# Kernel tuning notes

Measured on AMD Instinct MI355X. Metric: run time of the kernel, lower is better.

## Reference

```python
import jax, jax.numpy as jnp
import numpy as np

B = 2048      # env batch (graphs)
A = 8         # agents per graph (fully connected)
N = B * A     # total nodes
DIN = 192     # raw obs dim
HD = 256      # h_dim (base MLP)
MD = 256      # mem_dim (GRU)
GD = 128      # gnn_dim (per-head GATv2 out, concat=False -> head mean)
H = 4         # GAT heads
NA = 20       # n_actions
ED = 3        # edge_dim


def setup_inputs() -> dict:
    key = jax.random.key(0)
    ks = jax.random.split(key, 16)
    # fully-connected directed graph per group of A agents, no self loops
    s, d = np.meshgrid(np.arange(A), np.arange(A), indexing='ij')
    mask = s != d
    s = s[mask]; d = d[mask]                     # [A*(A-1)]
    off = (np.arange(B) * A)[:, None]
    src = (off + s[None, :]).reshape(-1)
    dst = (off + d[None, :]).reshape(-1)
    edge_index = jnp.asarray(np.stack([src, dst]), dtype=jnp.int32)  # [2, E]
    E = src.shape[0]
    p = lambda k, sh: jax.random.normal(ks[k], sh, jnp.float32) * 0.02
    return {
        'inputs': jax.random.normal(ks[0], (N, DIN), jnp.float32),
        'hidden_states': jax.random.normal(ks[1], (N, MD), jnp.float32) * 0.1,
        'edge_index': edge_index,
        'edge_attr': jax.random.uniform(ks[2], (E, ED), jnp.float32),
        # base MLP (2 layers: Linear+ReLU+LayerNorm)
        'W1': p(3, (DIN, HD)), 'b1': jnp.zeros(HD), 'g1': jnp.ones(HD), 'be1': jnp.zeros(HD),
        'W2': p(4, (HD, HD)),  'b2': jnp.zeros(HD), 'g2': jnp.ones(HD), 'be2': jnp.zeros(HD),
        # GRUCell
        'Wih': p(5, (3 * MD, HD)), 'Whh': p(6, (3 * MD, MD)),
        'bih': jnp.zeros(3 * MD), 'bhh': jnp.zeros(3 * MD),
        # GATv2Conv (edge_dim=3, heads=4, concat=False, residual)
        'Wl': p(7, (MD, H * GD)), 'bl': jnp.zeros(H * GD),
        'Wr': p(8, (MD, H * GD)), 'br': jnp.zeros(H * GD),
        'att': p(9, (H, GD)),
        'We': p(10, (ED, H * GD)),
        'Wres': p(11, (MD, GD)),
        'bg': jnp.zeros(GD),
        # head: LayerNorm + Linear
        'lng': jnp.ones(GD), 'lnb': jnp.zeros(GD),
        'Wout': p(12, (GD, NA)), 'bout': jnp.zeros(NA),
    }


def _ln(x, g, b):
    mu = jnp.mean(x, -1, keepdims=True)
    xc = x - mu
    v = jnp.mean(xc * xc, -1, keepdims=True)
    return xc * jax.lax.rsqrt(v + 1e-5) * g + b


def _fwd(inputs, hidden_states, edge_attr, edge_index,
         W1, b1, g1, be1, W2, b2, g2, be2,
         Wih, Whh, bih, bhh,
         Wl, bl, Wr, br, att, We, Wres, bg,
         lng, lnb, Wout, bout):
    src, dst = edge_index[0], edge_index[1]
    # ---- base MLP encode ----
    x = _ln(jax.nn.relu(inputs @ W1 + b1), g1, be1)
    x = _ln(jax.nn.relu(x @ W2 + b2), g2, be2)          # [N, HD]
    # ---- SimpleConv(aggr='mean', combine_root='self_loop') ----
    s = jax.ops.segment_sum(x[src], dst, num_segments=N) + x
    deg = jax.ops.segment_sum(jnp.ones(src.shape[0], x.dtype), dst, num_segments=N) + 1.0
    x = s / deg[:, None]                                 # [N, HD]
    # ---- GRUCell ----
    gi = x @ Wih.T + bih
    gh = hidden_states @ Whh.T + bhh
    ir, iz, inn = jnp.split(gi, 3, -1)
    hr, hz, hn = jnp.split(gh, 3, -1)
    r = jax.nn.sigmoid(ir + hr)
    z = jax.nn.sigmoid(iz + hz)
    n = jnp.tanh(inn + r * hn)
    h = (1.0 - z) * n + z * hidden_states                # [N, MD]
    # ---- GATv2Conv (add self loops, edge_attr fill='mean') ----
    loop = jnp.arange(N, dtype=src.dtype)
    sf = jnp.concatenate([src, loop])
    df = jnp.concatenate([dst, loop])
    ea = jnp.concatenate([edge_attr, jnp.broadcast_to(edge_attr.mean(0), (N, ED))], 0)
    xl = (h @ Wl + bl).reshape(N, H, GD)
    xr = (h @ Wr + br).reshape(N, H, GD)
    m = xl[sf] + xr[df] + (ea @ We).reshape(-1, H, GD)   # [Ef, H, GD]
    m = jnp.where(m > 0, m, 0.2 * m)                     # leaky_relu(0.2)
    logits = jnp.einsum('ehc,hc->eh', m, att)            # [Ef, H]
    mx = jax.ops.segment_max(logits, df, num_segments=N)
    ex = jnp.exp(logits - mx[df])
    den = jax.ops.segment_sum(ex, df, num_segments=N)
    alpha = ex / (den[df] + 1e-16)                       # segment softmax
    out = jax.ops.segment_sum(xl[sf] * alpha[..., None], df, num_segments=N)
    out = out.mean(1) + h @ Wres + bg                    # head mean + residual + bias
    zg = jax.nn.relu(out)                                # [N, GD]
    # ---- action head ----
    q = _ln(zg, lng, lnb) @ Wout + bout                  # [N, NA]
    return q, h


def reference(inputs, hidden_states, edge_index, edge_attr,
              W1, b1, g1, be1, W2, b2, g2, be2,
              Wih, Whh, bih, bhh,
              Wl, bl, Wr, br, att, We, Wres, bg,
              lng, lnb, Wout, bout):
    return _fwd(inputs, hidden_states, edge_attr, edge_index,
                W1, b1, g1, be1, W2, b2, g2, be2,
                Wih, Whh, bih, bhh,
                Wl, bl, Wr, br, att, We, Wres, bg,
                lng, lnb, Wout, bout)
```

## Files before the change

### kernel.cpp

```cpp
#include <hip/hip_runtime.h>
#include <hip/hip_bf16.h>

constexpr int NB  = 2048;
constexpr int AG  = 8;
constexpr int NN  = NB * AG;
constexpr int DIN = 192;
constexpr int HD  = 256;
constexpr int MD  = 256;
constexpr int GD  = 128;
constexpr int NA  = 20;
constexpr int NE  = NB * AG * (AG - 1);

typedef __attribute__((ext_vector_type(8))) short bfrag8;
typedef __attribute__((ext_vector_type(4))) float f32x4;

#define MFMA16(a, b, c) __builtin_amdgcn_mfma_f32_16x16x32_bf16((a), (b), (c), 0, 0, 0)

__device__ __forceinline__ float bf2f(__hip_bfloat16 x) { return __bfloat162float(x); }
__device__ __forceinline__ __hip_bfloat16 f2bf(float x) { return __float2bfloat16(x); }
__device__ __forceinline__ short f2bs(float x) {
    __hip_bfloat16 b = __float2bfloat16(x);
    return *reinterpret_cast<short*>(&b);
}
__device__ __forceinline__ bfrag8 ldf(const __hip_bfloat16* p) { return *(const bfrag8*)p; }
__device__ __forceinline__ bfrag8 ldf32(const float* p) {
    const f32x4 a = *(const f32x4*)p;
    const f32x4 b = *(const f32x4*)(p + 4);
    bfrag8 r;
    r[0] = f2bs(a[0]); r[1] = f2bs(a[1]); r[2] = f2bs(a[2]); r[3] = f2bs(a[3]);
    r[4] = f2bs(b[0]); r[5] = f2bs(b[1]); r[6] = f2bs(b[2]); r[7] = f2bs(b[3]);
    return r;
}
__device__ __forceinline__ float sigmf(float x) { return 1.f / (1.f + __expf(-x)); }
__device__ __forceinline__ float blo(unsigned u) { return __uint_as_float(u << 16); }
__device__ __forceinline__ float bhi(unsigned u) { return __uint_as_float(u & 0xffff0000u); }

__global__ __launch_bounds__(256) void k_prep(
    const float* __restrict__ W1, const float* __restrict__ W2,
    const float* __restrict__ Wih, const float* __restrict__ Whh,
    const float* __restrict__ Wl, const float* __restrict__ bl,
    const float* __restrict__ Wr, const float* __restrict__ br,
    const float* __restrict__ Wres, const float* __restrict__ Wout,
    __hip_bfloat16* __restrict__ W1T, __hip_bfloat16* __restrict__ W2T,
    __hip_bfloat16* __restrict__ WihB, __hip_bfloat16* __restrict__ WhhB,
    __hip_bfloat16* __restrict__ WcatT, float* __restrict__ WoutTf,
    float* __restrict__ bcat)
{
    int i = blockIdx.x * 256 + threadIdx.x;
    if (i < 49152) { int o = i / 192, c = i % 192; W1T[i] = f2bf(W1[c * 256 + o]); return; }
    i -= 49152;
    if (i < 65536) { int o = i >> 8, c = i & 255; W2T[i] = f2bf(W2[c * 256 + o]); return; }
    i -= 65536;
    if (i < 196608) { WihB[i] = f2bf(Wih[i]); return; }
    i -= 196608;
    if (i < 196608) { WhhB[i] = f2bf(Whh[i]); return; }
    i -= 196608;
    if (i < 294912) {
        int o = i >> 8, c = i & 255;
        float v;
        if (o < 512)       v = Wl[c * 512 + o];
        else if (o < 1024) v = Wr[c * 512 + (o - 512)];
        else               v = Wres[c * 128 + (o - 1024)];
        WcatT[i] = f2bf(v); return;
    }
    i -= 294912;
    if (i < 2560) { int o = i >> 7, c = i & 127; WoutTf[i] = Wout[c * 20 + o]; return; }
    i -= 2560;
    if (i < 1152) {
        float v = 0.f;
        if (i < 512) v = bl[i]; else if (i < 1024) v = br[i - 512];
        bcat[i] = v;
    }
}

__global__ __launch_bounds__(256) void k_easum1(const float* __restrict__ ea,
                                                float* __restrict__ partials)
{
    __shared__ float sw[4][3];
    const int b = blockIdx.x, tid = threadIdx.x;
    float a0 = 0.f, a1 = 0.f, a2 = 0.f;
#pragma unroll
    for (int k = 0; k < 7; k++) {
        int e = b * 1792 + k * 256 + tid;
        a0 += ea[e * 3 + 0];
        a1 += ea[e * 3 + 1];
        a2 += ea[e * 3 + 2];
    }
#pragma unroll
    for (int off = 1; off < 64; off <<= 1) {
        a0 += __shfl_xor(a0, off); a1 += __shfl_xor(a1, off); a2 += __shfl_xor(a2, off);
    }
    if ((tid & 63) == 0) { sw[tid >> 6][0] = a0; sw[tid >> 6][1] = a1; sw[tid >> 6][2] = a2; }
    __syncthreads();
    if (tid == 0) {
        partials[b * 3 + 0] = sw[0][0] + sw[1][0] + sw[2][0] + sw[3][0];
        partials[b * 3 + 1] = sw[0][1] + sw[1][1] + sw[2][1] + sw[3][1];
        partials[b * 3 + 2] = sw[0][2] + sw[1][2] + sw[2][2] + sw[3][2];
    }
}

__global__ void k_easum2(const float* __restrict__ partials, float* __restrict__ ea_mean)
{
    int t = threadIdx.x;
    if (t < 3) {
        float s = 0.f;
        for (int i = 0; i < 64; i++) s += partials[i * 3 + t];
        ea_mean[t] = s * (1.f / NE);
    }
}

__global__ __launch_bounds__(256) void k_encode(
    const float* __restrict__ in,
    const __hip_bfloat16* __restrict__ W1T,
    const float* __restrict__ b1, const float* __restrict__ g1, const float* __restrict__ be1,
    const __hip_bfloat16* __restrict__ W2T,
    const float* __restrict__ b2, const float* __restrict__ g2, const float* __restrict__ be2,
    __hip_bfloat16* __restrict__ xm)
{
    __shared__ float sf[16][257];
    __shared__ alignas(16) __hip_bfloat16 sb[16][264];
    const int tid = threadIdx.x;
    const int lane = tid & 63, w = tid >> 6;
    const int r = lane & 15, q = lane >> 4;
    const int m0 = blockIdx.x * 16;

    f32x4 acc[4];
#pragma unroll
    for (int i = 0; i < 4; i++) acc[i] = (f32x4){0.f, 0.f, 0.f, 0.f};

    {
        const float* ap = in + (size_t)(m0 + r) * DIN + q * 8;
#pragma unroll
        for (int kb = 0; kb < 6; kb++) {
            bfrag8 af = ldf32(ap + kb * 32);
#pragma unroll
            for (int i = 0; i < 4; i++) {
                int t = w * 4 + i;
                bfrag8 bfv = ldf(W1T + (size_t)(t * 16 + r) * DIN + kb * 32 + q * 8);
                acc[i] = MFMA16(af, bfv, acc[i]);
            }
        }
    }
#pragma unroll
    for (int i = 0; i < 4; i++) {
        int col = (w * 4 + i) * 16 + r;
        float bias = b1[col];
#pragma unroll
        for (int reg = 0; reg < 4; reg++)
            sf[q * 4 + reg][col] = fmaxf(acc[i][reg] + bias, 0.f);
    }
    __syncthreads();
    {
        int rowi = tid >> 4, c16 = tid & 15;
        float vals[16]; float s = 0.f, s2 = 0.f;
#pragma unroll
        for (int j = 0; j < 16; j++) { float v = sf[rowi][c16 + 16 * j]; vals[j] = v; s += v; s2 += v * v; }
#pragma unroll
        for (int off = 1; off < 16; off <<= 1) { s += __shfl_xor(s, off); s2 += __shfl_xor(s2, off); }
        float mean = s * (1.f / HD);
        float var = fmaxf(s2 * (1.f / HD) - mean * mean, 0.f);
        float rs = rsqrtf(var + 1e-5f);
#pragma unroll
        for (int j = 0; j < 16; j++) {
            int col = c16 + 16 * j;
            sb[rowi][col] = f2bf((vals[j] - mean) * rs * g1[col] + be1[col]);
        }
    }
    __syncthreads();

#pragma unroll
    for (int i = 0; i < 4; i++) acc[i] = (f32x4){0.f, 0.f, 0.f, 0.f};
    {
        const __hip_bfloat16* ap = &sb[r][0];
#pragma unroll
        for (int kb = 0; kb < 8; kb++) {
            bfrag8 af = ldf(ap + kb * 32 + q * 8);
#pragma unroll
            for (int i = 0; i < 4; i++) {
                int t = w * 4 + i;
                bfrag8 bfv = ldf(W2T + (size_t)(t * 16 + r) * HD + kb * 32 + q * 8);
                acc[i] = MFMA16(af, bfv, acc[i]);
            }
        }
    }
    __syncthreads();
#pragma unroll
    for (int i = 0; i < 4; i++) {
        int col = (w * 4 + i) * 16 + r;
        float bias = b2[col];
#pragma unroll
        for (int reg = 0; reg < 4; reg++)
            sf[q * 4 + reg][col] = fmaxf(acc[i][reg] + bias, 0.f);
    }
    __syncthreads();
    {
        int rowi = tid >> 4, c16 = tid & 15;
        float vals[16]; float s = 0.f, s2 = 0.f;
#pragma unroll
        for (int j = 0; j < 16; j++) { float v = sf[rowi][c16 + 16 * j]; vals[j] = v; s += v; s2 += v * v; }
#pragma unroll
        for (int off = 1; off < 16; off <<= 1) { s += __shfl_xor(s, off); s2 += __shfl_xor(s2, off); }
        float mean = s * (1.f / HD);
        float var = fmaxf(s2 * (1.f / HD) - mean * mean, 0.f);
        float rs = rsqrtf(var + 1e-5f);
#pragma unroll
        for (int j = 0; j < 16; j++) {
            int col = c16 + 16 * j;
            sb[rowi][col] = f2bf((vals[j] - mean) * rs * g2[col] + be2[col]);
        }
    }
    __syncthreads();
    {
        int col = tid;
        float a0 = 0.f, a1 = 0.f;
#pragma unroll
        for (int i = 0; i < 8; i++) { a0 += bf2f(sb[i][col]); a1 += bf2f(sb[8 + i][col]); }
        xm[(size_t)(2 * blockIdx.x) * HD + col] = f2bf(a0 * 0.125f);
        xm[(size_t)(2 * blockIdx.x + 1) * HD + col] = f2bf(a1 * 0.125f);
    }
}

__global__ __launch_bounds__(256) void k_gi(
    const __hip_bfloat16* __restrict__ xm,
    const __hip_bfloat16* __restrict__ WihB,
    const float* __restrict__ bih,
    float* __restrict__ gi)
{
    const int tid = threadIdx.x;
    const int lane = tid & 63, w = tid >> 6;
    const int r = lane & 15, q = lane >> 4;
    const int m0 = blockIdx.x * 16;

    f32x4 acc[12];
#pragma unroll
    for (int i = 0; i < 12; i++) acc[i] = (f32x4){0.f, 0.f, 0.f, 0.f};
    const __hip_bfloat16* ap = xm + (size_t)(m0 + r) * MD + q * 8;
#pragma unroll
    for (int kb = 0; kb < 8; kb++) {
        bfrag8 af = ldf(ap + kb * 32);
#pragma unroll
        for (int i = 0; i < 12; i++) {
            int t = w * 12 + i;
            bfrag8 bfv = ldf(WihB + (size_t)(t * 16 + r) * MD + kb * 32 + q * 8);
            acc[i] = MFMA16(af, bfv, acc[i]);
        }
    }
#pragma unroll
    for (int i = 0; i < 12; i++) {
        int col = (w * 12 + i) * 16 + r;
        float bias = bih[col];
#pragma unroll
        for (int reg = 0; reg < 4; reg++) {
            int R = m0 + q * 4 + reg;
            gi[(size_t)R * 768 + col] = acc[i][reg] + bias;
        }
    }
}

__global__ __launch_bounds__(256) void k_gru(
    const float* __restrict__ hprev,
    const __hip_bfloat16* __restrict__ WhhB,
    const float* __restrict__ bhh,
    const float* __restrict__ gi,
    float* __restrict__ hout)
{
    const int tid = threadIdx.x;
    const int lane = tid & 63, w = tid >> 6;
    const int r = lane & 15, q = lane >> 4;
    const int m0 = blockIdx.x * 16;

    f32x4 aR[4], aZ[4], aN[4];
#pragma unroll
    for (int i = 0; i < 4; i++) {
        aR[i] = (f32x4){0.f, 0.f, 0.f, 0.f};
        aZ[i] = (f32x4){0.f, 0.f, 0.f, 0.f};
        aN[i] = (f32x4){0.f, 0.f, 0.f, 0.f};
    }
    const float* ap = hprev + (size_t)(m0 + r) * MD + q * 8;
#pragma unroll
    for (int kb = 0; kb < 8; kb++) {
        bfrag8 af = ldf32(ap + kb * 32);
#pragma unroll
        for (int i = 0; i < 4; i++) {
            int ct = w * 4 + i;
            bfrag8 bR = ldf(WhhB + (size_t)(ct * 16 + r) * MD + kb * 32 + q * 8);
            bfrag8 bZ = ldf(WhhB + (size_t)(256 + ct * 16 + r) * MD + kb * 32 + q * 8);
            bfrag8 bN = ldf(WhhB + (size_t)(512 + ct * 16 + r) * MD + kb * 32 + q * 8);
            aR[i] = MFMA16(af, bR, aR[i]);
            aZ[i] = MFMA16(af, bZ, aZ[i]);
            aN[i] = MFMA16(af, bN, aN[i]);
        }
    }
#pragma unroll
    for (int i = 0; i < 4; i++) {
        int c = (w * 4 + i) * 16 + r;
        float bhr = bhh[c], bhz = bhh[256 + c], bhn = bhh[512 + c];
#pragma unroll
        for (int reg = 0; reg < 4; reg++) {
            int R = m0 + q * 4 + reg;
            const float* gir = gi + (size_t)(R >> 3) * 768;
            float rr = sigmf(gir[c] + aR[i][reg] + bhr);
            float zz = sigmf(gir[256 + c] + aZ[i][reg] + bhz);
            float nn = tanhf(gir[512 + c] + rr * (aN[i][reg] + bhn));
            float hp = hprev[(size_t)R * MD + c];
            hout[(size_t)R * MD + c] = (1.f - zz) * nn + zz * hp;
        }
    }
}

__global__ __launch_bounds__(256, 3) void k_gat(
    const float* __restrict__ h,
    const __hip_bfloat16* __restrict__ WcatT,
    const float* __restrict__ bcat,
    const float* __restrict__ ea,
    const float* __restrict__ ea_mean,
    const float* __restrict__ att,
    const float* __restrict__ We,
    const float* __restrict__ bg,
    const float* __restrict__ lng, const float* __restrict__ lnb,
    const float* __restrict__ WoutTf,
    const float* __restrict__ bout,
    float* __restrict__ qout)
{
    __shared__ __hip_bfloat16 sx[16][1160];
    __shared__ float slog[2][4][8][8];
    __shared__ __hip_bfloat16 satt[4][128];
    __shared__ __hip_bfloat16 sWe[3][512];
    __shared__ float szg[16][129];
    __shared__ float sea[2][56][3];
    const int tid = threadIdx.x;
    const int lane = tid & 63, w = tid >> 6;
    const int r = lane & 15, q = lane >> 4;
    const int m0 = blockIdx.x * 16;

    for (int idx = tid; idx < 512; idx += 256) satt[idx >> 7][idx & 127] = f2bf(att[idx]);
    for (int idx = tid; idx < 1536; idx += 256) sWe[idx / 512][idx % 512] = f2bf(We[idx]);
    if (tid < 112) {
        int gg = tid / 56, e = tid % 56;
        int g2 = blockIdx.x * 2 + gg;
        sea[gg][e][0] = ea[(size_t)(g2 * 56 + e) * 3 + 0];
        sea[gg][e][1] = ea[(size_t)(g2 * 56 + e) * 3 + 1];
        sea[gg][e][2] = ea[(size_t)(g2 * 56 + e) * 3 + 2];
    }

#pragma unroll
    for (int pass = 0; pass < 2; pass++) {
        bfrag8 afr[8];
        const float* ap = h + (size_t)(m0 + r) * MD + q * 8;
#pragma unroll
        for (int kb = 0; kb < 8; kb++) afr[kb] = ldf32(ap + kb * 32);
        f32x4 acc[9];
#pragma unroll
        for (int i = 0; i < 9; i++) acc[i] = (f32x4){0.f, 0.f, 0.f, 0.f};
#pragma unroll
        for (int kb = 0; kb < 8; kb++) {
#pragma unroll
            for (int i = 0; i < 9; i++) {
                int t = pass * 36 + w * 9 + i;
                bfrag8 bfv = ldf(WcatT + (size_t)(t * 16 + r) * MD + kb * 32 + q * 8);
                acc[i] = MFMA16(afr[kb], bfv, acc[i]);
            }
        }
#pragma unroll
        for (int i = 0; i < 9; i++) {
            int col = (pass * 36 + w * 9 + i) * 16 + r;
            float bias = bcat[col];
#pragma unroll
            for (int reg = 0; reg < 4; reg++)
                sx[q * 4 + reg][col] = f2bf(acc[i][reg] + bias);
        }
    }
    __syncthreads();

    {
        const int gg = w >> 1;
        const int s = lane >> 3, d = lane & 7;
        const float em0 = ea_mean[0], em1 = ea_mean[1], em2 = ea_mean[2];
        float e0, e1, e2;
        if (s == d) { e0 = em0; e1 = em1; e2 = em2; }
        else {
            int el = s * 7 + d - (d > s ? 1 : 0);
            e0 = sea[gg][el][0]; e1 = sea[gg][el][1]; e2 = sea[gg][el][2];
        }
#pragma unroll
        for (int hi = 0; hi < 2; hi++) {
            const int hh = (w & 1) + hi * 2;
            const unsigned* xl = (const unsigned*)&sx[gg * 8 + s][hh * 128];
            const unsigned* xr = (const unsigned*)&sx[gg * 8 + d][512 + hh * 128];
            const unsigned* w0 = (const unsigned*)&sWe[0][hh * 128];
            const unsigned* w1 = (const unsigned*)&sWe[1][hh * 128];
            const unsigned* w2 = (const unsigned*)&sWe[2][hh * 128];
            const unsigned* at = (const unsigned*)&satt[hh][0];
            float accl = 0.f;
#pragma unroll 8
            for (int c2 = 0; c2 < 64; c2++) {
                unsigned uxl = xl[c2], uxr = xr[c2];
                unsigned uw0 = w0[c2], uw1 = w1[c2], uw2 = w2[c2], uat = at[c2];
                float m0v = blo(uxl) + blo(uxr) + e0 * blo(uw0) + e1 * blo(uw1) + e2 * blo(uw2);
                m0v = (m0v > 0.f) ? m0v : 0.2f * m0v;
                accl = fmaf(m0v, blo(uat), accl);
                float m1v = bhi(uxl) + bhi(uxr) + e0 * bhi(uw0) + e1 * bhi(uw1) + e2 * bhi(uw2);
                m1v = (m1v > 0.f) ? m1v : 0.2f * m1v;
                accl = fmaf(m1v, bhi(uat), accl);
            }
            slog[gg][hh][d][s] = accl;
        }
    }
    __syncthreads();

    if (tid < 64) {
        int gg = tid >> 5, hh = (tid >> 3) & 3, d = tid & 7;
        float* L = &slog[gg][hh][d][0];
        float mx = L[0];
#pragma unroll
        for (int s = 1; s < 8; s++) mx = fmaxf(mx, L[s]);
        float ex[8]; float den = 0.f;
#pragma unroll
        for (int s = 0; s < 8; s++) { ex[s] = __expf(L[s] - mx); den += ex[s]; }
        float inv = 1.f / (den + 1e-16f);
#pragma unroll
        for (int s = 0; s < 8; s++) L[s] = ex[s] * inv;
    }
    __syncthreads();

    {
        f32x4 acc0 = (f32x4){0.f, 0.f, 0.f, 0.f};
        f32x4 acc1 = (f32x4){0.f, 0.f, 0.f, 0.f};
        const int ggr = r >> 3, dr = r & 7;
#pragma unroll
        for (int hh = 0; hh < 4; hh++) {
            bfrag8 afA;
#pragma unroll
            for (int j = 0; j < 8; j++) {
                int k = q * 8 + j;
                float v = 0.f;
                if (k < 16) {
                    int ggk = k >> 3, s = k & 7;
                    if (ggk == ggr) v = slog[ggk][hh][dr][s];
                }
                afA[j] = f2bs(v);
            }
#pragma unroll
            for (int j2 = 0; j2 < 2; j2++) {
                int chunk = w * 2 + j2;
                bfrag8 bfB;
#pragma unroll
                for (int j = 0; j < 8; j++) {
                    int k = (q * 8 + j) & 15;
                    bfB[j] = *(const short*)&sx[k][hh * 128 + chunk * 16 + r];
                }
                if (j2 == 0) acc0 = MFMA16(afA, bfB, acc0);
                else         acc1 = MFMA16(afA, bfB, acc1);
            }
        }
#pragma unroll
        for (int j2 = 0; j2 < 2; j2++) {
            f32x4 a = j2 ? acc1 : acc0;
            int c = (w * 2 + j2) * 16 + r;
            float bgc = bg[c];
#pragma unroll
            for (int reg = 0; reg < 4; reg++) {
                int row = q * 4 + reg;
                float o = a[reg] * 0.25f + bf2f(sx[row][1024 + c]) + bgc;
                szg[row][c] = fmaxf(o, 0.f);
            }
        }
    }
    __syncthreads();

    {
        int row = tid >> 4, j = tid & 15;
        float v[8]; float s = 0.f, s2 = 0.f;
#pragma unroll
        for (int cj = 0; cj < 8; cj++) { v[cj] = szg[row][j + 16 * cj]; s += v[cj]; s2 += v[cj] * v[cj]; }
#pragma unroll
        for (int off = 1; off < 16; off <<= 1) { s += __shfl_xor(s, off); s2 += __shfl_xor(s2, off); }
        float mean = s * (1.f / GD);
        float var = fmaxf(s2 * (1.f / GD) - mean * mean, 0.f);
        float rs = rsqrtf(var + 1e-5f);
#pragma unroll
        for (int cj = 0; cj < 8; cj++) {
            int c = j + 16 * cj;
            szg[row][c] = (v[cj] - mean) * rs * lng[c] + lnb[c];
        }
    }
    __syncthreads();

    {
        int row = tid >> 4, j = tid & 15;
        for (int jj = j; jj < NA; jj += 16) {
            float a = bout[jj];
            const float* wo = WoutTf + jj * 128;
            for (int c = 0; c < 128; c++) a = fmaf(szg[row][c], wo[c], a);
            qout[(size_t)(m0 + row) * NA + jj] = a;
        }
    }
}

extern "C" void kernel_launch(void* const* d_in, const int* in_sizes, int n_in,
                              void* d_out, int out_size, void* d_ws, size_t ws_size,
                              hipStream_t stream) {
    const float* inp   = (const float*)d_in[0];
    const float* hid   = (const float*)d_in[1];
    const float* eatt  = (const float*)d_in[3];
    const float* W1    = (const float*)d_in[4];
    const float* b1    = (const float*)d_in[5];
    const float* g1    = (const float*)d_in[6];
    const float* be1   = (const float*)d_in[7];
    const float* W2    = (const float*)d_in[8];
    const float* b2    = (const float*)d_in[9];
    const float* g2    = (const float*)d_in[10];
    const float* be2   = (const float*)d_in[11];
    const float* Wih   = (const float*)d_in[12];
    const float* Whh   = (const float*)d_in[13];
    const float* bih   = (const float*)d_in[14];
    const float* bhh   = (const float*)d_in[15];
    const float* Wl    = (const float*)d_in[16];
    const float* bl    = (const float*)d_in[17];
    const float* Wr    = (const float*)d_in[18];
    const float* br    = (const float*)d_in[19];
    const float* att   = (const float*)d_in[20];
    const float* We    = (const float*)d_in[21];
    const float* Wres  = (const float*)d_in[22];
    const float* bg    = (const float*)d_in[23];
    const float* lng   = (const float*)d_in[24];
    const float* lnb   = (const float*)d_in[25];
    const float* Wout  = (const float*)d_in[26];
    const float* bout  = (const float*)d_in[27];

    float* qout = (float*)d_out;
    float* hout = (float*)d_out + (size_t)NN * NA;

    char* ws = (char*)d_ws;
    float*           ea_partials = (float*)ws;
    float*           ea_mean     = (float*)(ws + 1024);
    __hip_bfloat16*  xm    = (__hip_bfloat16*)(ws + 2048);
    float*           gi    = (float*)(ws + 1050624);
    __hip_bfloat16*  W1T   = (__hip_bfloat16*)(ws + 7342080);
    __hip_bfloat16*  W2T   = (__hip_bfloat16*)(ws + 7440384);
    __hip_bfloat16*  WihB  = (__hip_bfloat16*)(ws + 7571456);
    __hip_bfloat16*  WhhB  = (__hip_bfloat16*)(ws + 7964672);
    __hip_bfloat16*  WcatT = (__hip_bfloat16*)(ws + 8357888);
    float*           bcat  = (float*)(ws + 8947712);
    float*           WoutTf= (float*)(ws + 8952320);

    k_easum1<<<64, 256, 0, stream>>>(eatt, ea_partials);
    k_easum2<<<1, 64, 0, stream>>>(ea_partials, ea_mean);
    k_prep<<<3151, 256, 0, stream>>>(W1, W2, Wih, Whh, Wl, bl, Wr, br, Wres, Wout,
                                     W1T, W2T, WihB, WhhB, WcatT, WoutTf, bcat);
    k_encode<<<NN / 16, 256, 0, stream>>>(inp, W1T, b1, g1, be1, W2T, b2, g2, be2, xm);
    k_gi<<<NB / 16, 256, 0, stream>>>(xm, WihB, bih, gi);
    k_gru<<<NN / 16, 256, 0, stream>>>(hid, WhhB, bhh, gi, hout);
    k_gat<<<NN / 16, 256, 0, stream>>>(hout, WcatT, bcat, eatt, ea_mean, att, We, bg,
                                       lng, lnb, WoutTf, bout, qout);
}
```

Measured before the change: 369.4 us.

## Restructure GAT logit computation across lanes and vectorize LDS stores in k_gat

The projection MFMA swaps its operands so each lane holds four consecutive output columns, which lets the bias-add results go to shared memory as one packed 8-byte store instead of scalar stores. The per-edge attention logits are rebuilt so each lane handles four channels of a (group, head) pair, with cross-lane shuffle reductions and edge attributes kept in registers and broadcast by shuffles, replacing the serial 128-channel loop per thread and the shared edge-attribute buffer. The output head reads szg and Wout as float4 with a padded row stride. This adds many shuffles per logit and some extra register pressure in exchange for fewer LDS accesses and more parallel work per logit.

After: 363.6 us. About the same (-1.6%).

```diff
diff --git a/kernel.cpp b/kernel.cpp
--- a/kernel.cpp
+++ b/kernel.cpp
@@ -12,6 +12,7 @@
 constexpr int NE  = NB * AG * (AG - 1);
 
 typedef __attribute__((ext_vector_type(8))) short bfrag8;
+typedef __attribute__((ext_vector_type(4))) short sfrag4;
 typedef __attribute__((ext_vector_type(4))) float f32x4;
 
 #define MFMA16(a, b, c) __builtin_amdgcn_mfma_f32_16x16x32_bf16((a), (b), (c), 0, 0, 0)
@@ -322,12 +323,11 @@
     const float* __restrict__ bout,
     float* __restrict__ qout)
 {
-    __shared__ __hip_bfloat16 sx[16][1160];
+    __shared__ alignas(16) __hip_bfloat16 sx[16][1160];
     __shared__ float slog[2][4][8][8];
-    __shared__ __hip_bfloat16 satt[4][128];
-    __shared__ __hip_bfloat16 sWe[3][512];
-    __shared__ float szg[16][129];
-    __shared__ float sea[2][56][3];
+    __shared__ alignas(16) __hip_bfloat16 satt[4][128];
+    __shared__ alignas(16) __hip_bfloat16 sWe[3][512];
+    __shared__ alignas(16) float szg[16][132];
     const int tid = threadIdx.x;
     const int lane = tid & 63, w = tid >> 6;
     const int r = lane & 15, q = lane >> 4;
@@ -335,82 +335,109 @@
 
     for (int idx = tid; idx < 512; idx += 256) satt[idx >> 7][idx & 127] = f2bf(att[idx]);
     for (int idx = tid; idx < 1536; idx += 256) sWe[idx / 512][idx % 512] = f2bf(We[idx]);
-    if (tid < 112) {
-        int gg = tid / 56, e = tid % 56;
-        int g2 = blockIdx.x * 2 + gg;
-        sea[gg][e][0] = ea[(size_t)(g2 * 56 + e) * 3 + 0];
-        sea[gg][e][1] = ea[(size_t)(g2 * 56 + e) * 3 + 1];
-        sea[gg][e][2] = ea[(size_t)(g2 * 56 + e) * 3 + 2];
-    }
-
-#pragma unroll
-    for (int pass = 0; pass < 2; pass++) {
+
+    float vea[2][3];
+    {
+        int l = (lane < 56) ? lane : 0;
+#pragma unroll
+        for (int g = 0; g < 2; g++) {
+            const float* ep = ea + (size_t)((blockIdx.x * 2 + g) * 56 + l) * 3;
+            vea[g][0] = ep[0]; vea[g][1] = ep[1]; vea[g][2] = ep[2];
+        }
+    }
+    const float em0 = ea_mean[0], em1 = ea_mean[1], em2 = ea_mean[2];
+
+    {
         bfrag8 afr[8];
         const float* ap = h + (size_t)(m0 + r) * MD + q * 8;
 #pragma unroll
         for (int kb = 0; kb < 8; kb++) afr[kb] = ldf32(ap + kb * 32);
-        f32x4 acc[9];
-#pragma unroll
-        for (int i = 0; i < 9; i++) acc[i] = (f32x4){0.f, 0.f, 0.f, 0.f};
-#pragma unroll
-        for (int kb = 0; kb < 8; kb++) {
+#pragma unroll
+        for (int pass = 0; pass < 2; pass++) {
+            f32x4 acc[9];
+#pragma unroll
+            for (int i = 0; i < 9; i++) acc[i] = (f32x4){0.f, 0.f, 0.f, 0.f};
+#pragma unroll
+            for (int kb = 0; kb < 8; kb++) {
+#pragma unroll
+                for (int i = 0; i < 9; i++) {
+                    int t = pass * 36 + w * 9 + i;
+                    bfrag8 bfv = ldf(WcatT + (size_t)(t * 16 + r) * MD + kb * 32 + q * 8);
+                    acc[i] = MFMA16(bfv, afr[kb], acc[i]);
+                }
+            }
 #pragma unroll
             for (int i = 0; i < 9; i++) {
-                int t = pass * 36 + w * 9 + i;
-                bfrag8 bfv = ldf(WcatT + (size_t)(t * 16 + r) * MD + kb * 32 + q * 8);
-                acc[i] = MFMA16(afr[kb], bfv, acc[i]);
-            }
-        }
-#pragma unroll
-        for (int i = 0; i < 9; i++) {
-            int col = (pass * 36 + w * 9 + i) * 16 + r;
-            float bias = bcat[col];
-#pragma unroll
-            for (int reg = 0; reg < 4; reg++)
-                sx[q * 4 + reg][col] = f2bf(acc[i][reg] + bias);
-        }
-    }
-    __syncthreads();
-
-    {
-        const int gg = w >> 1;
-        const int s = lane >> 3, d = lane & 7;
-        const float em0 = ea_mean[0], em1 = ea_mean[1], em2 = ea_mean[2];
-        float e0, e1, e2;
-        if (s == d) { e0 = em0; e1 = em1; e2 = em2; }
-        else {
-            int el = s * 7 + d - (d > s ? 1 : 0);
-            e0 = sea[gg][el][0]; e1 = sea[gg][el][1]; e2 = sea[gg][el][2];
-        }
-#pragma unroll
-        for (int hi = 0; hi < 2; hi++) {
-            const int hh = (w & 1) + hi * 2;
-            const unsigned* xl = (const unsigned*)&sx[gg * 8 + s][hh * 128];
-            const unsigned* xr = (const unsigned*)&sx[gg * 8 + d][512 + hh * 128];
-            const unsigned* w0 = (const unsigned*)&sWe[0][hh * 128];
-            const unsigned* w1 = (const unsigned*)&sWe[1][hh * 128];
-            const unsigned* w2 = (const unsigned*)&sWe[2][hh * 128];
-            const unsigned* at = (const unsigned*)&satt[hh][0];
-            float accl = 0.f;
-#pragma unroll 8
-            for (int c2 = 0; c2 < 64; c2++) {
-                unsigned uxl = xl[c2], uxr = xr[c2];
-                unsigned uw0 = w0[c2], uw1 = w1[c2], uw2 = w2[c2], uat = at[c2];
-                float m0v = blo(uxl) + blo(uxr) + e0 * blo(uw0) + e1 * blo(uw1) + e2 * blo(uw2);
-                m0v = (m0v > 0.f) ? m0v : 0.2f * m0v;
-                accl = fmaf(m0v, blo(uat), accl);
-                float m1v = bhi(uxl) + bhi(uxr) + e0 * bhi(uw0) + e1 * bhi(uw1) + e2 * bhi(uw2);
-                m1v = (m1v > 0.f) ? m1v : 0.2f * m1v;
-                accl = fmaf(m1v, bhi(uat), accl);
-            }
-            slog[gg][hh][d][s] = accl;
+                int fbase = (pass * 36 + w * 9 + i) * 16 + q * 4;
+                sfrag4 pk;
+#pragma unroll
+                for (int reg = 0; reg < 4; reg++)
+                    pk[reg] = f2bs(acc[i][reg] + bcat[fbase + reg]);
+                *(sfrag4*)&sx[r][fbase] = pk;
+            }
+        }
+    }
+    __syncthreads();
+
+    {
+        const int li = lane & 31, half = lane >> 5;
+#pragma unroll
+        for (int t = 0; t < 2; t++) {
+            const int combo = w * 2 + t;
+            const int gg = combo >> 2, hh = combo & 3;
+            uint2 uat = *(const uint2*)&satt[hh][li * 4];
+            uint2 u0  = *(const uint2*)&sWe[0][hh * 128 + li * 4];
+            uint2 u1  = *(const uint2*)&sWe[1][hh * 128 + li * 4];
+            uint2 u2  = *(const uint2*)&sWe[2][hh * 128 + li * 4];
+            float at0 = blo(uat.x), at1 = bhi(uat.x), at2 = blo(uat.y), at3 = bhi(uat.y);
+            float w00 = blo(u0.x),  w01 = bhi(u0.x),  w02 = blo(u0.y),  w03 = bhi(u0.y);
+            float w10 = blo(u1.x),  w11 = bhi(u1.x),  w12 = blo(u1.y),  w13 = bhi(u1.y);
+            float w20 = blo(u2.x),  w21 = bhi(u2.x),  w22 = blo(u2.y),  w23 = bhi(u2.y);
+            float ve0 = vea[gg][0], ve1 = vea[gg][1], ve2 = vea[gg][2];
+            float xv[4][4];
+#pragma unroll
+            for (int sh = 0; sh < 4; sh++) {
+                int sL = sh * 2 + half;
+                uint2 uxl = *(const uint2*)&sx[gg * 8 + sL][hh * 128 + li * 4];
+                xv[sh][0] = blo(uxl.x); xv[sh][1] = bhi(uxl.x);
+                xv[sh][2] = blo(uxl.y); xv[sh][3] = bhi(uxl.y);
+            }
+            float mylog = 0.f;
+#pragma unroll
+            for (int d = 0; d < 8; d++) {
+                uint2 uxr = *(const uint2*)&sx[gg * 8 + d][512 + hh * 128 + li * 4];
+                float xr0 = blo(uxr.x), xr1 = bhi(uxr.x), xr2 = blo(uxr.y), xr3 = bhi(uxr.y);
+#pragma unroll
+                for (int sh = 0; sh < 4; sh++) {
+                    int sL = sh * 2 + half;
+                    int el = sL * 7 + d - (d > sL ? 1 : 0);
+                    float e0 = __shfl(ve0, el), e1 = __shfl(ve1, el), e2 = __shfl(ve2, el);
+                    bool slf = (sL == d);
+                    e0 = slf ? em0 : e0; e1 = slf ? em1 : e1; e2 = slf ? em2 : e2;
+                    float p, m;
+                    m = fmaf(e2, w20, fmaf(e1, w10, fmaf(e0, w00, xv[sh][0]))) + xr0;
+                    m = fmaxf(m, 0.2f * m); p = m * at0;
+                    m = fmaf(e2, w21, fmaf(e1, w11, fmaf(e0, w01, xv[sh][1]))) + xr1;
+                    m = fmaxf(m, 0.2f * m); p = fmaf(m, at1, p);
+                    m = fmaf(e2, w22, fmaf(e1, w12, fmaf(e0, w02, xv[sh][2]))) + xr2;
+                    m = fmaxf(m, 0.2f * m); p = fmaf(m, at2, p);
+                    m = fmaf(e2, w23, fmaf(e1, w13, fmaf(e0, w03, xv[sh][3]))) + xr3;
+                    m = fmaxf(m, 0.2f * m); p = fmaf(m, at3, p);
+                    p += __shfl_xor(p, 1);  p += __shfl_xor(p, 2);  p += __shfl_xor(p, 4);
+                    p += __shfl_xor(p, 8);  p += __shfl_xor(p, 16);
+                    float got = __shfl(p, ((lane & 1) << 5) | li);
+                    bool want = ((lane >> 3) == d) && (((lane & 7) >> 1) == sh);
+                    mylog = want ? got : mylog;
+                }
+            }
+            ((float*)&slog[gg][hh][0][0])[lane] = mylog;
         }
     }
     __syncthreads();
 
     if (tid < 64) {
-        int gg = tid >> 5, hh = (tid >> 3) & 3, d = tid & 7;
-        float* L = &slog[gg][hh][d][0];
+        int sg = tid >> 5, sh = (tid >> 3) & 3, d = tid & 7;
+        float* L = &slog[sg][sh][d][0];
         float mx = L[0];
 #pragma unroll
         for (int s = 1; s < 8; s++) mx = fmaxf(mx, L[s]);
@@ -428,7 +455,7 @@
         f32x4 acc1 = (f32x4){0.f, 0.f, 0.f, 0.f};
         const int ggr = r >> 3, dr = r & 7;
 #pragma unroll
-        for (int hh = 0; hh < 4; hh++) {
+        for (int ah = 0; ah < 4; ah++) {
             bfrag8 afA;
 #pragma unroll
             for (int j = 0; j < 8; j++) {
@@ -436,7 +463,7 @@
                 float v = 0.f;
                 if (k < 16) {
                     int ggk = k >> 3, s = k & 7;
-                    if (ggk == ggr) v = slog[ggk][hh][dr][s];
+                    if (ggk == ggr) v = slog[ggk][ah][dr][s];
                 }
                 afA[j] = f2bs(v);
             }
@@ -447,7 +474,7 @@
 #pragma unroll
                 for (int j = 0; j < 8; j++) {
                     int k = (q * 8 + j) & 15;
-                    bfB[j] = *(const short*)&sx[k][hh * 128 + chunk * 16 + r];
+                    bfB[j] = *(const short*)&sx[k][ah * 128 + chunk * 16 + r];
                 }
                 if (j2 == 0) acc0 = MFMA16(afA, bfB, acc0);
                 else         acc1 = MFMA16(afA, bfB, acc1);
@@ -491,7 +518,13 @@
         for (int jj = j; jj < NA; jj += 16) {
             float a = bout[jj];
             const float* wo = WoutTf + jj * 128;
-            for (int c = 0; c < 128; c++) a = fmaf(szg[row][c], wo[c], a);
+#pragma unroll
+            for (int c4 = 0; c4 < 32; c4++) {
+                f32x4 z = *(const f32x4*)&szg[row][c4 * 4];
+                const f32x4 wv = *(const f32x4*)&wo[c4 * 4];
+                a = fmaf(z[0], wv[0], a); a = fmaf(z[1], wv[1], a);
+                a = fmaf(z[2], wv[2], a); a = fmaf(z[3], wv[3], a);
+            }
             qout[(size_t)(m0 + row) * NA + jj] = a;
         }
     }
```
